# Optimization experiments

Hardware: AMD Instinct MI355X
Metric: run time of the kernel (lower is better)

## Reference

```python
import jax, jax.numpy as jnp
import numpy as np

IN_CH, OUT_CH, KS = 64, 128, 3
GRID, DEG = 8, 3
STRIDE, PAD = 1, 1
SIZE = IN_CH * KS * KS            # 576
NCOEF = GRID + DEG                # 11
GRID_RANGE = (-1.0, 1.0)


def _xavier_uniform(key, shape):
    fan_out, fan_in = shape
    a = float(np.sqrt(6.0 / (fan_in + fan_out)))
    return jax.random.uniform(key, shape, minval=-a, maxval=a, dtype=jnp.float32)


def setup_inputs() -> dict:
    key = jax.random.key(0)
    k1, k2, k3 = jax.random.split(key, 3)
    x = jax.random.normal(k1, (8, IN_CH, 32, 32), dtype=jnp.float32)
    # non-trainable knot grid, one row per unfolded feature
    knots = jnp.tile(jnp.linspace(GRID_RANGE[0], GRID_RANGE[1], GRID + 1, dtype=jnp.float32)[None, :], (SIZE, 1))
    coeff = 0.1 * jax.random.normal(k2, (OUT_CH, SIZE, NCOEF), dtype=jnp.float32)
    base_weights = _xavier_uniform(k3, (OUT_CH, SIZE))
    spline_weights = jnp.ones((OUT_CH, SIZE), dtype=jnp.float32)
    return {"x": x, "knots": knots, "coeff": coeff,
            "base_weights": base_weights, "spline_weights": spline_weights}


def bspline_basis(x, grid, k):
    # x: (S, P) evaluation points; grid: (S, G+1) knots. Returns (S, G+k, P).
    h = (grid[:, -1:] - grid[:, :1]) / (grid.shape[1] - 1)
    left = grid[:, :1] - h * jnp.arange(k, 0, -1, dtype=x.dtype)
    right = grid[:, -1:] + h * jnp.arange(1, k + 1, dtype=x.dtype)
    g = jnp.concatenate([left, grid, right], axis=1)  # (S, G+1+2k)
    xe = x[:, None, :]
    B = ((xe >= g[:, :-1, None]) & (xe < g[:, 1:, None])).astype(x.dtype)
    for d in range(1, k + 1):  # de Boor recursion over fixed degree
        B = ((xe - g[:, :-(d + 1), None]) / (g[:, d:-1, None] - g[:, :-(d + 1), None]) * B[:, :-1]
             + (g[:, d + 1:, None] - xe) / (g[:, d + 1:, None] - g[:, 1:-d, None]) * B[:, 1:])
    return B


def _unfold(x):
    # torch F.unfold with channel-major (c, kh, kw) feature ordering
    N, C, H, W = x.shape
    xp = jnp.pad(x, ((0, 0), (0, 0), (PAD, PAD), (PAD, PAD)))
    Hp = (H + 2 * PAD - KS) // STRIDE + 1
    Wp = (W + 2 * PAD - KS) // STRIDE + 1
    patches = jnp.stack([xp[:, :, i:i + STRIDE * Hp:STRIDE, j:j + STRIDE * Wp:STRIDE]
                         for i in range(KS) for j in range(KS)], axis=2)  # (N, C, KS*KS, Hp, Wp)
    L = Hp * Wp
    u = patches.reshape(N, SIZE, L)              # (N, size, L)
    u = jnp.transpose(u, (1, 0, 2)).reshape(SIZE, N * L)  # (size, N*L), col = n*L + l
    return u, Hp, Wp


def reference(x, knots, coeff, base_weights, spline_weights):
    N = x.shape[0]
    u, Hp, Wp = _unfold(x)                                   # (size, P)
    base = base_weights @ jax.nn.silu(u)                     # (Cout, P)
    B = bspline_basis(u, knots, DEG)                         # (size, ncoef, P)
    eff = spline_weights[:, :, None] * coeff                 # (Cout, size, ncoef)
    spl = jnp.einsum('csj,sjp->cp', eff, B)                  # (Cout, P)
    out = (base + spl).reshape(OUT_CH, N, Hp, Wp)
    return jnp.transpose(out, (1, 0, 2, 3))                  # (N, Cout, Hp, Wp)
```

## Files before the change

kernel.cpp:

```cpp
#include <hip/hip_runtime.h>


typedef __attribute__((ext_vector_type(8))) short bf16x8;
typedef __attribute__((ext_vector_type(4))) float f32x4;
typedef __attribute__((ext_vector_type(16))) float f32x16;
typedef __attribute__((ext_vector_type(4))) unsigned short u16x4;

#define WSWZ_BYTES 1769472
#define PHI_OFF    WSWZ_BYTES
#define PHI_BYTES  14205696
#define PART_OFF   (PHI_OFF + PHI_BYTES)

__device__ __forceinline__ short f2bf(float f) {
    union { float f; unsigned u; } c; c.f = f;
    unsigned r = c.u + 0x7fffu + ((c.u >> 16) & 1u);
    return (short)(r >> 16);
}
__device__ __forceinline__ float bf2f(unsigned short u) {
    union { unsigned u; float f; } c; c.u = ((unsigned)u) << 16;
    return c.f;
}

__global__ void kan_prep(const float* __restrict__ coeff,
                         const float* __restrict__ basew,
                         const float* __restrict__ splw,
                         const float* __restrict__ x,
                         short* __restrict__ Wswz,
                         short* __restrict__ Phi) {
    __shared__ float coeffL[6336];
    __shared__ float basewL[576];
    __shared__ float splwL[576];
    __shared__ unsigned short xs[64 * 32];
    const int t = threadIdx.x;

    if (blockIdx.x < 272) {
        const int rowid = blockIdx.x;
        const int n     = rowid / 34;
        const int ypad  = rowid - n * 34;
        const int y     = ypad - 1;
        const bool yvalid = (y >= 0 && y < 32);

        if (yvalid) {
#pragma unroll
            for (int it = 0; it < 2; ++it) {
                int cg = t + it * 256;
                int ci = cg >> 3, q = cg & 7;
                f32x4 v = *(const f32x4*)(x + (((n * 64 + ci) * 32 + y) * 32 + q * 4));
                u16x4 p;
                p.x = (unsigned short)f2bf(v.x); p.y = (unsigned short)f2bf(v.y);
                p.z = (unsigned short)f2bf(v.z); p.w = (unsigned short)f2bf(v.w);
                *(u16x4*)&xs[ci * 32 + q * 4] = p;
            }
        }
        __syncthreads();

        const size_t rowbase = (size_t)rowid * 12 * 2176;
        for (int it = t; it < 272; it += 256) {
            int xp = it >> 3, cch = it & 7, c0 = cch << 3;
            bool interior = yvalid && (xp >= 1 && xp <= 32);
            int px = xp - 1;
            int pxc = px < 0 ? 0 : (px > 31 ? 31 : px);
            bf16x8 packs[12];
#pragma unroll
            for (int j = 0; j < 8; ++j) {
                float v = interior ? bf2f(xs[(c0 + j) * 32 + pxc]) : 0.f;
                float tt = 4.f * v + 7.f;
                int   i0 = -100;
                float b0 = 0.f, b1 = 0.f, b2 = 0.f, b3 = 0.f;
                if (tt >= 0.f && tt < 14.f) {
                    i0 = (int)tt;
                    float fr  = tt - (float)i0;
                    float omf = 1.f - fr;
                    float fr2 = fr * fr, fr3 = fr2 * fr;
                    b0 = omf * omf * omf * (1.f / 6.f);
                    b1 = (3.f * fr3 - 6.f * fr2 + 4.f) * (1.f / 6.f);
                    b2 = (-3.f * fr3 + 3.f * fr2 + 3.f * fr + 1.f) * (1.f / 6.f);
                    b3 = fr3 * (1.f / 6.f);
                }
                float silu = v * __builtin_amdgcn_rcpf(1.f + __expf(-v));
                packs[0][j] = f2bf(silu);
#pragma unroll
                for (int f = 1; f < 12; ++f) {
                    int jj = f - 1;
                    float val = 0.f;
                    val = (jj == i0 - 3) ? b0 : val;
                    val = (jj == i0 - 2) ? b1 : val;
                    val = (jj == i0 - 1) ? b2 : val;
                    val = (jj == i0    ) ? b3 : val;
                    packs[f][j] = f2bf(val);
                }
            }
            int swz = (cch ^ (xp & 7)) << 3;
#pragma unroll
            for (int f = 0; f < 12; ++f)
                *(bf16x8*)&Phi[rowbase + (size_t)f * 2176 + xp * 64 + swz] = packs[f];
        }
    } else {
        const int co = blockIdx.x - 272;
        const float* crow = coeff + co * 6336;
        for (int i = t; i < 6336; i += 256) coeffL[i] = crow[i];
        for (int i = t; i < 576; i += 256) {
            basewL[i] = basew[co * 576 + i];
            splwL[i]  = splw[co * 576 + i];
        }
        __syncthreads();
        const int cb = co >> 5, lm = co & 31;
        for (int c = t; c < 864; c += 256) {
            int kk16 = c >> 1, kh = c & 1;
            int f  = kk16 / 36;
            int rm = kk16 - f * 36;
            int tap = rm >> 2, q = rm & 3;
            bf16x8 pack;
#pragma unroll
            for (int j = 0; j < 8; ++j) {
                int ci = q * 16 + kh * 8 + j;
                int s  = ci * 9 + tap;
                float v = (f == 0) ? basewL[s] : splwL[s] * coeffL[s * 11 + (f - 1)];
                pack[j] = f2bf(v);
            }
            *(bf16x8*)(Wswz + (size_t)((kk16 * 4 + cb) * 64 + kh * 32 + lm) * 8) = pack;
        }
    }
}

__global__ __launch_bounds__(256, 4)
void kan_gemm(const short* __restrict__ Phi,
              const short* __restrict__ Wswz,
              float* __restrict__ part) {
    __shared__ short Bs[2 * 8704];

    const int t  = threadIdx.x;
    const int w  = t >> 6;
    const int l  = t & 63;
    const int ln = l & 31;
    const int kh = l >> 5;

    const int fg    = blockIdx.x >> 7;
    const int ptile = blockIdx.x & 127;
    const int n     = ptile >> 4;
    const int y0    = (ptile & 15) << 1;

    const char* phiB = (const char*)Phi;
    const int planeBase = (n * 34 + y0) * 12 + fg * 2;
#pragma unroll
    for (int k = 0; k < 9; ++k) {
        int i = t + k * 256;
        if (i < 2176) {
            int pl  = i / 1088;
            int r2  = i - pl * 1088;
            int row = r2 / 272;
            int m   = r2 - row * 272;
            const char* s = phiB + (size_t)(planeBase + row * 12 + pl) * 4352 + m * 16;
            auto gsrc = (const __attribute__((address_space(1))) unsigned int*)s;
            auto ldst = (__attribute__((address_space(3))) unsigned int*)((char*)&Bs[0] + i * 16);
            __builtin_amdgcn_global_load_lds(gsrc, ldst, 16, 0, 0);
        }
    }
    __syncthreads();

    f32x16 acc[2];
#pragma unroll
    for (int pb = 0; pb < 2; ++pb)
#pragma unroll
        for (int r = 0; r < 16; ++r)
            acc[pb][r] = 0.f;

    const short* Abase = Wswz + (size_t)w * 512 + (size_t)l * 8;
    __builtin_amdgcn_s_setprio(1);
#pragma unroll
    for (int p = 0; p < 2; ++p) {
        const short* B0 = Bs + p * 8704;
        const int kbase = (fg * 2 + p) * 36;
#pragma unroll
        for (int q = 0; q < 4; ++q) {
#pragma unroll
            for (int dx = 0; dx < 3; ++dx) {
                bf16x8 a0 = *(const bf16x8*)(Abase + (size_t)(kbase + (0 * 3 + dx) * 4 + q) * 2048);
                bf16x8 a1 = *(const bf16x8*)(Abase + (size_t)(kbase + (1 * 3 + dx) * 4 + q) * 2048);
                bf16x8 a2 = *(const bf16x8*)(Abase + (size_t)(kbase + (2 * 3 + dx) * 4 + q) * 2048);
                const int c   = q * 2 + kh;
                const int key = (ln + dx) & 7;
                bf16x8 b0, b1, b2, b3;
                {
                    int pix0 = 0 * 34 + ln + dx;
                    int pix1 = 1 * 34 + ln + dx;
                    int pix2 = 2 * 34 + ln + dx;
                    int pix3 = 3 * 34 + ln + dx;
                    int slot = (c ^ key) << 3;
                    b0 = *(const bf16x8*)&B0[pix0 * 64 + slot];
                    b1 = *(const bf16x8*)&B0[pix1 * 64 + slot];
                    b2 = *(const bf16x8*)&B0[pix2 * 64 + slot];
                    b3 = *(const bf16x8*)&B0[pix3 * 64 + slot];
                }
                acc[0] = __builtin_amdgcn_mfma_f32_32x32x16_bf16(a0, b0, acc[0], 0, 0, 0);
                acc[1] = __builtin_amdgcn_mfma_f32_32x32x16_bf16(a0, b1, acc[1], 0, 0, 0);
                acc[0] = __builtin_amdgcn_mfma_f32_32x32x16_bf16(a1, b1, acc[0], 0, 0, 0);
                acc[1] = __builtin_amdgcn_mfma_f32_32x32x16_bf16(a1, b2, acc[1], 0, 0, 0);
                acc[0] = __builtin_amdgcn_mfma_f32_32x32x16_bf16(a2, b2, acc[0], 0, 0, 0);
                acc[1] = __builtin_amdgcn_mfma_f32_32x32x16_bf16(a2, b3, acc[1], 0, 0, 0);
            }
        }
    }
    __builtin_amdgcn_s_setprio(0);

    float* dst = part + (size_t)fg * 1048576;
#pragma unroll
    for (int pb = 0; pb < 2; ++pb) {
        int y = y0 + pb;
#pragma unroll
        for (int r = 0; r < 16; ++r) {
            int row = (r & 3) + 8 * (r >> 2) + 4 * kh;
            int co  = w * 32 + row;
            dst[((size_t)(n * 128 + co) * 32 + y) * 32 + ln] = acc[pb][r];
        }
    }
}

__global__ void kan_reduce(const float* __restrict__ part,
                           float* __restrict__ out) {
    const int r = blockIdx.x;
    const int p = r & 127;
    const int i = r >> 7;
    const int n  = p >> 4;
    const int yp = p & 15;
    const int c  = i * 256 + threadIdx.x;
    const int co = c >> 4;
    const int rem = c & 15;
    const int yy = rem >> 3, xq = rem & 7;
    const size_t idx = ((size_t)(n * 128 + co) * 32 + yp * 2 + yy) * 8 + xq;
    f32x4 a = ((const f32x4*)part)[idx];
#pragma unroll
    for (int s = 1; s < 6; ++s)
        a += ((const f32x4*)(part + (size_t)s * 1048576))[idx];
    ((f32x4*)out)[idx] = a;
}

extern "C" void kernel_launch(void* const* d_in, const int* in_sizes, int n_in,
                              void* d_out, int out_size, void* d_ws, size_t ws_size,
                              hipStream_t stream) {
    const float* x     = (const float*)d_in[0];
    const float* coeff = (const float*)d_in[2];
    const float* basew = (const float*)d_in[3];
    const float* splw  = (const float*)d_in[4];
    float* out = (float*)d_out;

    short* Wswz = (short*)d_ws;
    short* Phi  = (short*)((char*)d_ws + PHI_OFF);
    float* part = (float*)((char*)d_ws + PART_OFF);

    kan_prep<<<400, 256, 0, stream>>>(coeff, basew, splw, x, Wswz, Phi);
    kan_gemm<<<768, 256, 0, stream>>>(Phi, Wswz, part);
    kan_reduce<<<1024, 256, 0, stream>>>(part, out);
}
```

Before: 112.5 us.

## Split GEMM K-planes across 8 waves with LDS reduction and preloaded A fragments

The GEMM block doubles to 512 threads. Each half of the waves processes one of the two feature planes rather than one wave iterating over both, and the two partial accumulators are combined through LDS before the store. All 36 A-operand fragments are loaded into registers up front, overlapping the global-to-LDS Phi copy, instead of being fetched inside the MFMA loop. This shortens the serial MFMA chain per wave and hides weight-load latency. In exchange it raises register pressure (36 bf16x8 vectors plus accumulators), adds an extra LDS round trip and barrier, and drops the setprio hints.

```diff
diff --git a/kernel.cpp b/kernel.cpp
--- a/kernel.cpp
+++ b/kernel.cpp
@@ -123,14 +123,16 @@
     }
 }
 
-__global__ __launch_bounds__(256, 4)
+__global__ __launch_bounds__(512, 2)
 void kan_gemm(const short* __restrict__ Phi,
               const short* __restrict__ Wswz,
               float* __restrict__ part) {
     __shared__ short Bs[2 * 8704];
 
     const int t  = threadIdx.x;
-    const int w  = t >> 6;
+    const int w8 = t >> 6;
+    const int cb = w8 & 3;
+    const int p  = w8 >> 2;
     const int l  = t & 63;
     const int ln = l & 31;
     const int kh = l >> 5;
@@ -143,19 +145,33 @@
     const char* phiB = (const char*)Phi;
     const int planeBase = (n * 34 + y0) * 12 + fg * 2;
 #pragma unroll
-    for (int k = 0; k < 9; ++k) {
-        int i = t + k * 256;
+    for (int k = 0; k < 5; ++k) {
+        int i = t + k * 512;
         if (i < 2176) {
             int pl  = i / 1088;
             int r2  = i - pl * 1088;
             int row = r2 / 272;
             int m   = r2 - row * 272;
             const char* s = phiB + (size_t)(planeBase + row * 12 + pl) * 4352 + m * 16;
-            auto gsrc = (const __attribute__((address_space(1))) unsigned int*)s;
-            auto ldst = (__attribute__((address_space(3))) unsigned int*)((char*)&Bs[0] + i * 16);
-            __builtin_amdgcn_global_load_lds(gsrc, ldst, 16, 0, 0);
-        }
-    }
+            __builtin_amdgcn_global_load_lds(
+                (const __attribute__((address_space(1))) unsigned int*)s,
+                (__attribute__((address_space(3))) unsigned int*)((char*)Bs + i * 16),
+                16, 0, 0);
+        }
+    }
+
+    const int kbase = (fg * 2 + p) * 36;
+    const short* Abase = Wswz + (size_t)cb * 512 + (size_t)l * 8;
+    bf16x8 ag[36];
+#pragma unroll
+    for (int g = 0; g < 36; ++g) {
+        int q  = g / 9;
+        int r9 = g - q * 9;
+        int dx = r9 / 3;
+        int dy = r9 - dx * 3;
+        ag[g] = *(const bf16x8*)(Abase + (size_t)(kbase + (dy * 3 + dx) * 4 + q) * 2048);
+    }
+
     __syncthreads();
 
     f32x16 acc[2];
@@ -165,53 +181,59 @@
         for (int r = 0; r < 16; ++r)
             acc[pb][r] = 0.f;
 
-    const short* Abase = Wswz + (size_t)w * 512 + (size_t)l * 8;
-    __builtin_amdgcn_s_setprio(1);
-#pragma unroll
-    for (int p = 0; p < 2; ++p) {
-        const short* B0 = Bs + p * 8704;
-        const int kbase = (fg * 2 + p) * 36;
-#pragma unroll
-        for (int q = 0; q < 4; ++q) {
-#pragma unroll
-            for (int dx = 0; dx < 3; ++dx) {
-                bf16x8 a0 = *(const bf16x8*)(Abase + (size_t)(kbase + (0 * 3 + dx) * 4 + q) * 2048);
-                bf16x8 a1 = *(const bf16x8*)(Abase + (size_t)(kbase + (1 * 3 + dx) * 4 + q) * 2048);
-                bf16x8 a2 = *(const bf16x8*)(Abase + (size_t)(kbase + (2 * 3 + dx) * 4 + q) * 2048);
-                const int c   = q * 2 + kh;
-                const int key = (ln + dx) & 7;
-                bf16x8 b0, b1, b2, b3;
-                {
-                    int pix0 = 0 * 34 + ln + dx;
-                    int pix1 = 1 * 34 + ln + dx;
-                    int pix2 = 2 * 34 + ln + dx;
-                    int pix3 = 3 * 34 + ln + dx;
-                    int slot = (c ^ key) << 3;
-                    b0 = *(const bf16x8*)&B0[pix0 * 64 + slot];
-                    b1 = *(const bf16x8*)&B0[pix1 * 64 + slot];
-                    b2 = *(const bf16x8*)&B0[pix2 * 64 + slot];
-                    b3 = *(const bf16x8*)&B0[pix3 * 64 + slot];
-                }
-                acc[0] = __builtin_amdgcn_mfma_f32_32x32x16_bf16(a0, b0, acc[0], 0, 0, 0);
-                acc[1] = __builtin_amdgcn_mfma_f32_32x32x16_bf16(a0, b1, acc[1], 0, 0, 0);
-                acc[0] = __builtin_amdgcn_mfma_f32_32x32x16_bf16(a1, b1, acc[0], 0, 0, 0);
-                acc[1] = __builtin_amdgcn_mfma_f32_32x32x16_bf16(a1, b2, acc[1], 0, 0, 0);
-                acc[0] = __builtin_amdgcn_mfma_f32_32x32x16_bf16(a2, b2, acc[0], 0, 0, 0);
-                acc[1] = __builtin_amdgcn_mfma_f32_32x32x16_bf16(a2, b3, acc[1], 0, 0, 0);
-            }
-        }
-    }
-    __builtin_amdgcn_s_setprio(0);
-
-    float* dst = part + (size_t)fg * 1048576;
-#pragma unroll
-    for (int pb = 0; pb < 2; ++pb) {
-        int y = y0 + pb;
-#pragma unroll
-        for (int r = 0; r < 16; ++r) {
-            int row = (r & 3) + 8 * (r >> 2) + 4 * kh;
-            int co  = w * 32 + row;
-            dst[((size_t)(n * 128 + co) * 32 + y) * 32 + ln] = acc[pb][r];
+    const short* B0 = Bs + p * 8704;
+#pragma unroll
+    for (int q = 0; q < 4; ++q) {
+#pragma unroll
+        for (int dx = 0; dx < 3; ++dx) {
+            const int g0 = (q * 3 + dx) * 3;
+            const int c   = q * 2 + kh;
+            const int key = (ln + dx) & 7;
+            const int colb = (ln + dx) * 64 + ((c ^ key) << 3);
+            bf16x8 b0 = *(const bf16x8*)&B0[0 * 2176 + colb];
+            bf16x8 b1 = *(const bf16x8*)&B0[1 * 2176 + colb];
+            bf16x8 b2 = *(const bf16x8*)&B0[2 * 2176 + colb];
+            bf16x8 b3 = *(const bf16x8*)&B0[3 * 2176 + colb];
+            acc[0] = __builtin_amdgcn_mfma_f32_32x32x16_bf16(ag[g0 + 0], b0, acc[0], 0, 0, 0);
+            acc[1] = __builtin_amdgcn_mfma_f32_32x32x16_bf16(ag[g0 + 0], b1, acc[1], 0, 0, 0);
+            acc[0] = __builtin_amdgcn_mfma_f32_32x32x16_bf16(ag[g0 + 1], b1, acc[0], 0, 0, 0);
+            acc[1] = __builtin_amdgcn_mfma_f32_32x32x16_bf16(ag[g0 + 1], b2, acc[1], 0, 0, 0);
+            acc[0] = __builtin_amdgcn_mfma_f32_32x32x16_bf16(ag[g0 + 2], b2, acc[0], 0, 0, 0);
+            acc[1] = __builtin_amdgcn_mfma_f32_32x32x16_bf16(ag[g0 + 2], b3, acc[1], 0, 0, 0);
+        }
+    }
+
+    __syncthreads();
+    float* ex = (float*)Bs;
+    if (p == 1) {
+#pragma unroll
+        for (int pb = 0; pb < 2; ++pb)
+#pragma unroll
+            for (int r = 0; r < 16; ++r) {
+                int v = pb * 16 + r;
+                ex[cb * 2048 + l * 32 + ((v + l) & 31)] = acc[pb][r];
+            }
+    }
+    __syncthreads();
+    if (p == 0) {
+#pragma unroll
+        for (int pb = 0; pb < 2; ++pb)
+#pragma unroll
+            for (int r = 0; r < 16; ++r) {
+                int v = pb * 16 + r;
+                acc[pb][r] += ex[cb * 2048 + l * 32 + ((v + l) & 31)];
+            }
+
+        float* dst = part + (size_t)fg * 1048576;
+#pragma unroll
+        for (int pb = 0; pb < 2; ++pb) {
+            int y = y0 + pb;
+#pragma unroll
+            for (int r = 0; r < 16; ++r) {
+                int row = (r & 3) + 8 * (r >> 2) + 4 * kh;
+                int co  = cb * 32 + row;
+                dst[((size_t)(n * 128 + co) * 32 + y) * 32 + ln] = acc[pb][r];
+            }
         }
     }
 }
@@ -249,6 +271,6 @@
     float* part = (float*)((char*)d_ws + PART_OFF);
 
     kan_prep<<<400, 256, 0, stream>>>(coeff, basew, splw, x, Wswz, Phi);
-    kan_gemm<<<768, 256, 0, stream>>>(Phi, Wswz, part);
+    kan_gemm<<<768, 512, 0, stream>>>(Phi, Wswz, part);
     kan_reduce<<<1024, 256, 0, stream>>>(part, out);
 }
```

After: 110.4 us. Within noise of the previous version (-1.9%).
